# Optimization experiments

Hardware: AMD Instinct MI355X
Metric: run time of the kernel (lower is better)

Reference implementation:

```python
import jax, jax.numpy as jnp
import numpy as np

DIM = 64; NH = 4; WS = (2, 7, 7); FRAMES = 8
# torch code uses head_dim = dim // num_heads for BOTH attentions' scale
SCALE = (DIM // NH) ** -0.5

def _rel_pos_index(ws):
    coords = np.stack(np.meshgrid(np.arange(ws[0]), np.arange(ws[1]), np.arange(ws[2]), indexing='ij'))
    cf = coords.reshape(3, -1)
    rc = (cf[:, :, None] - cf[:, None, :]).transpose(1, 2, 0)
    rc[:, :, 0] += ws[0] - 1; rc[:, :, 1] += ws[1] - 1; rc[:, :, 2] += ws[2] - 1
    rc[:, :, 0] *= (2 * ws[1] - 1) * (2 * ws[2] - 1)
    rc[:, :, 1] *= 2 * ws[2] - 1
    return jnp.asarray(rc.sum(-1))

REL_S = _rel_pos_index(WS)              # (98, 98)
REL_T = _rel_pos_index((FRAMES, 1, 1))  # (8, 8)

def _ln(x, g, b, eps=1e-5):
    m = x.mean(-1, keepdims=True)
    v = ((x - m) ** 2).mean(-1, keepdims=True)
    return (x - m) * jax.lax.rsqrt(v + eps) * g + b

def _conv3d(x, w, b):
    y = jax.lax.conv_general_dilated(x, w, (1, 1, 1), [(1, 1)] * 3,
                                     dimension_numbers=('NCDHW', 'OIDHW', 'NCDHW'))
    return y + b[None, :, None, None, None]

def setup_inputs():
    key = jax.random.key(0)
    ks = jax.random.split(key, 16)
    B, D, H, W, C = 2, 8, 112, 112, DIM
    C2 = C // 2
    n = lambda i, shape: jax.random.normal(ks[i], shape, jnp.float32) * 0.02
    return dict(
        x=jax.random.normal(ks[0], (B, D, H, W, C), jnp.float32),
        mask_matrix=jnp.zeros((1, 98, 98), jnp.float32),
        g1=jnp.ones((C,), jnp.float32), b1=jnp.zeros((C,), jnp.float32),
        rpb_s=n(1, ((2*WS[0]-1)*(2*WS[1]-1)*(2*WS[2]-1), NH)),
        qkv_w_s=n(2, (C, 3*C)), qkv_b_s=jnp.zeros((3*C,), jnp.float32),
        proj_w_s=n(3, (C, C)), proj_b_s=jnp.zeros((C,), jnp.float32),
        rpb_t=n(4, (2*FRAMES-1, NH)),
        qkv_w_t=n(5, (C, 3*C2)), qkv_b_t=jnp.zeros((3*C2,), jnp.float32),
        proj_w_t=n(6, (C2, C)), proj_b_t=jnp.zeros((C,), jnp.float32),
        g2=jnp.ones((C,), jnp.float32), b2=jnp.zeros((C,), jnp.float32),
        p1c1_w=n(7, (C2, C2, 3, 3, 3)), p1c1_b=jnp.zeros((C2,), jnp.float32),
        p1c2_w=n(8, (C2, C2, 3, 3, 3)), p1c2_b=jnp.zeros((C2,), jnp.float32),
        p2c1_w=n(9, (C2, C2, 3, 3, 3)), p2c1_b=jnp.zeros((C2,), jnp.float32),
        p2c2_w=n(10, (C2, C2, 3, 3, 3)), p2c2_b=jnp.zeros((C2,), jnp.float32),
    )

def reference(x, mask_matrix, g1, b1, rpb_s, qkv_w_s, qkv_b_s, proj_w_s, proj_b_s,
              rpb_t, qkv_w_t, qkv_b_t, proj_w_t, proj_b_t, g2, b2,
              p1c1_w, p1c1_b, p1c2_w, p1c2_b, p2c1_w, p2c1_b, p2c2_w, p2c2_b):
    B, D, H, W, C = x.shape
    C2 = C // 2
    wd, wh, ww = WS
    N = wd * wh * ww
    shortcut = x
    h = _ln(x, g1, b1)
    # ---- space attention over (2,7,7) windows (shift=0, H/W/D divisible -> no pad/roll/mask) ----
    xw = h.reshape(B, D // wd, wd, H // wh, wh, W // ww, ww, C)
    xw = xw.transpose(0, 1, 3, 5, 2, 4, 6, 7).reshape(-1, N, C)  # (nW, N, C)
    nw = xw.shape[0]
    qkv = (xw @ qkv_w_s + qkv_b_s).reshape(nw, N, 3, NH, C // NH).transpose(2, 0, 3, 1, 4)
    q, k, v = qkv[0] * SCALE, qkv[1], qkv[2]
    attn = jnp.einsum('whnd,whmd->whnm', q, k)
    bias = rpb_s[REL_S.reshape(-1)].reshape(N, N, NH).transpose(2, 0, 1)
    attn = jax.nn.softmax(attn + bias[None], axis=-1)
    out = jnp.einsum('whnm,whmd->whnd', attn, v).transpose(0, 2, 1, 3).reshape(nw, N, C)
    out = out @ proj_w_s + proj_b_s
    space = out.reshape(B, D // wd, H // wh, W // ww, wd, wh, ww, C)
    space = space.transpose(0, 1, 4, 2, 5, 3, 6, 7).reshape(B, D, H, W, C)
    # ---- time attention over frames (qkv projects to C/2) ----
    xt = h.transpose(0, 2, 3, 1, 4).reshape(B * H * W, D, C)
    qkv_t = (xt @ qkv_w_t + qkv_b_t).reshape(-1, D, 3, NH, C2 // NH).transpose(2, 0, 3, 1, 4)
    qt, kt, vt = qkv_t[0] * SCALE, qkv_t[1], qkv_t[2]
    at = jnp.einsum('bhnd,bhmd->bhnm', qt, kt)
    bias_t = rpb_t[REL_T.reshape(-1)].reshape(D, D, NH).transpose(2, 0, 1)
    at = jax.nn.softmax(at + bias_t[None], axis=-1)
    ot = jnp.einsum('bhnm,bhmd->bhnd', at, vt).transpose(0, 2, 1, 3).reshape(-1, D, C2)
    ot = ot @ proj_w_t + proj_b_t  # (B*H*W, D, C)
    time = ot.reshape(B, H, W, D, C).transpose(0, 3, 1, 2, 4)
    x = shortcut + time + space
    # ---- GRFFNet conv FFN ----
    h2 = _ln(x, g2, b2).transpose(0, 4, 1, 2, 3)  # (B,C,D,H,W)
    x1, x2 = h2[:, :C2], h2[:, C2:]
    y1 = x1 + _conv3d(jax.nn.leaky_relu(_conv3d(x1, p1c1_w, p1c1_b)), p1c2_w, p1c2_b)
    x2 = x2 + y1
    y2 = x2 + _conv3d(jax.nn.leaky_relu(_conv3d(x2, p2c1_w, p2c1_b)), p2c2_w, p2c2_b)
    y = jnp.concatenate([y1, y2], axis=1).transpose(0, 2, 3, 4, 1)
    return x + y
```

## Files before the change

### kernel.cpp

```cpp
#include <hip/hip_runtime.h>
#include <hip/hip_bf16.h>

typedef unsigned short u16;
typedef unsigned int u32;
typedef __attribute__((ext_vector_type(8))) short s16x8;
typedef __attribute__((ext_vector_type(4))) float f32x4;

__device__ __forceinline__ u16 f2b(float v) {
  u32 bits = __float_as_uint(v);
  bits += 0x7fffu + ((bits >> 16) & 1u);
  return (u16)(bits >> 16);
}
__device__ __forceinline__ float b2f(u16 u) { return __uint_as_float(((u32)u) << 16); }
__device__ __forceinline__ float bflo(u32 w) { return __uint_as_float(w << 16); }
__device__ __forceinline__ float bfhi(u32 w) { return __uint_as_float(w & 0xffff0000u); }

__global__ __launch_bounds__(256) void k_ln(const float* __restrict__ x, const float* __restrict__ g,
    const float* __restrict__ b, float* __restrict__ hout, u16* __restrict__ xb) {
  int token = blockIdx.x * 4 + (threadIdx.x >> 6);
  int lane = threadIdx.x & 63;
  long base = (long)token * 64 + lane;
  float v = x[base];
  float s = v;
#pragma unroll
  for (int o = 32; o; o >>= 1) s += __shfl_xor(s, o);
  float m = s * 0.015625f;
  float d = v - m;
  float q = d * d;
#pragma unroll
  for (int o = 32; o; o >>= 1) q += __shfl_xor(q, o);
  float r = rsqrtf(q * 0.015625f + 1e-5f);
  float hv = d * r * g[lane] + b[lane];
  hout[base] = hv;
  if (lane < 32) xb[(long)token * 32 + lane] = f2b(hv);
}

__global__ __launch_bounds__(256) void k_prep(const float* __restrict__ pw, u16* __restrict__ pwb,
    const float* __restrict__ tqw, u16* __restrict__ twb,
    const float* __restrict__ sqw, u16* __restrict__ swb,
    const float* __restrict__ rpb, float* __restrict__ Bt) {
  int i = blockIdx.x * 256 + threadIdx.x;
  if (i < 4096) {
    int r = i & 7, q = i >> 3;
    int col = q & 15; q >>= 4;
    int lk = q & 1; q >>= 1;
    int nt = q & 3, hd = q >> 2;
    pwb[i] = f2b(pw[(hd * 16 + lk * 8 + r) * 64 + nt * 16 + col]);
  } else if (i < 10240) {
    int j = i - 4096;
    int kk = j & 31, q = j >> 5;
    int lm = q & 15, ksnt = q >> 4;
    int ks = ksnt & 1, nt = ksnt >> 1;
    twb[j] = f2b(tqw[(ks * 32 + kk) * 96 + nt * 16 + lm]);
  } else if (i < 22528) {
    int j = i - 10240;
    int kk = j & 31, q = j >> 5;
    int lm = q & 15, ksnt = q >> 4;
    int ks = ksnt & 1, nt = ksnt >> 1;
    swb[j] = f2b(sqw[(ks * 32 + kk) * 192 + nt * 16 + lm]);
  } else {
    int j = i - 22528;
    int m = j % 112, q = j / 112;
    int n = q % 112, hd = q / 112;
    float v = -1e30f;
    if (n < 98 && m < 98) {
      int dzn = n / 49, rn = n % 49, hyn = rn / 7, wxn = rn % 7;
      int dzm = m / 49, rm = m % 49, hym = rm / 7, wxm = rm % 7;
      int idx = (dzn - dzm + 1) * 169 + (hyn - hym + 6) * 13 + (wxn - wxm + 6);
      v = rpb[idx * 4 + hd];
    }
    Bt[j] = v;
  }
}

__global__ __launch_bounds__(256) void k_wprep(const float* __restrict__ w0, const float* __restrict__ w1,
    const float* __restrict__ w2, const float* __restrict__ w3, u16* __restrict__ WB) {
  int j = blockIdx.x * 256 + threadIdx.x;
  int c = j / 27648, j2 = j - c * 27648;
  const float* src = c == 0 ? w0 : c == 1 ? w1 : c == 2 ? w2 : w3;
  int co = j2 / 864, rem = j2 - co * 864, ci = rem / 27, kk = rem - ci * 27;
  WB[c * 27648 + kk * 1024 + co * 32 + ci] = f2b(src[j2]);
}

__global__ __launch_bounds__(256) void k_fused1(const float* __restrict__ x,
    const float* __restrict__ g1, const float* __restrict__ b1,
    const u16* __restrict__ swb, const float* __restrict__ sqb,
    const u16* __restrict__ twb, const float* __restrict__ tqb,
    float* __restrict__ acc, u16* __restrict__ Qg, u16* __restrict__ Kg,
    u16* __restrict__ Vg, u16* __restrict__ T) {
  int l = threadIdx.x & 63, wv = threadIdx.x >> 6;
  int lm = l & 15, lk = l >> 4;
  long t0 = (long)blockIdx.x * 64 + wv * 16;
  long tok = t0 + lm;
  const float* xp = x + tok * 64 + lk * 8;
  float* ap = acc + tok * 64 + lk * 8;
  float va[16];
  float s = 0.f;
#pragma unroll
  for (int ks = 0; ks < 2; ks++) {
    float4 a0 = *(const float4*)(xp + ks * 32);
    float4 a1 = *(const float4*)(xp + ks * 32 + 4);
    *(float4*)(ap + ks * 32) = a0;
    *(float4*)(ap + ks * 32 + 4) = a1;
    va[ks * 8 + 0] = a0.x; va[ks * 8 + 1] = a0.y; va[ks * 8 + 2] = a0.z; va[ks * 8 + 3] = a0.w;
    va[ks * 8 + 4] = a1.x; va[ks * 8 + 5] = a1.y; va[ks * 8 + 6] = a1.z; va[ks * 8 + 7] = a1.w;
    s += a0.x + a0.y + a0.z + a0.w + a1.x + a1.y + a1.z + a1.w;
  }
  s += __shfl_xor(s, 16); s += __shfl_xor(s, 32);
  float m = s * 0.015625f;
  float q = 0.f;
#pragma unroll
  for (int j = 0; j < 16; j++) { float d = va[j] - m; q += d * d; }
  q += __shfl_xor(q, 16); q += __shfl_xor(q, 32);
  float r = rsqrtf(q * 0.015625f + 1e-5f);
  s16x8 A[2];
#pragma unroll
  for (int ks = 0; ks < 2; ks++) {
    float4 g0 = *(const float4*)(g1 + ks * 32 + lk * 8);
    float4 g4 = *(const float4*)(g1 + ks * 32 + lk * 8 + 4);
    float4 c0 = *(const float4*)(b1 + ks * 32 + lk * 8);
    float4 c4 = *(const float4*)(b1 + ks * 32 + lk * 8 + 4);
    s16x8 a;
    a[0] = (short)f2b((va[ks * 8 + 0] - m) * r * g0.x + c0.x);
    a[1] = (short)f2b((va[ks * 8 + 1] - m) * r * g0.y + c0.y);
    a[2] = (short)f2b((va[ks * 8 + 2] - m) * r * g0.z + c0.z);
    a[3] = (short)f2b((va[ks * 8 + 3] - m) * r * g0.w + c0.w);
    a[4] = (short)f2b((va[ks * 8 + 4] - m) * r * g4.x + c4.x);
    a[5] = (short)f2b((va[ks * 8 + 5] - m) * r * g4.y + c4.y);
    a[6] = (short)f2b((va[ks * 8 + 6] - m) * r * g4.z + c4.z);
    a[7] = (short)f2b((va[ks * 8 + 7] - m) * r * g4.w + c4.w);
    A[ks] = a;
  }
  f32x4 C[12], D[6];
#pragma unroll
  for (int nt = 0; nt < 12; nt++) C[nt] = (f32x4){0.f, 0.f, 0.f, 0.f};
#pragma unroll
  for (int nt = 0; nt < 6; nt++) D[nt] = (f32x4){0.f, 0.f, 0.f, 0.f};
#pragma unroll
  for (int ks = 0; ks < 2; ks++) {
#pragma unroll
    for (int nt = 0; nt < 12; nt++) {
      s16x8 B = *(const s16x8*)&swb[((nt * 2 + ks) * 16 + lm) * 32 + lk * 8];
      C[nt] = __builtin_amdgcn_mfma_f32_16x16x32_bf16(A[ks], B, C[nt], 0, 0, 0);
    }
#pragma unroll
    for (int nt = 0; nt < 6; nt++) {
      s16x8 B = *(const s16x8*)&twb[((nt * 2 + ks) * 16 + lm) * 32 + lk * 8];
      D[nt] = __builtin_amdgcn_mfma_f32_16x16x32_bf16(A[ks], B, D[nt], 0, 0, 0);
    }
  }
  float sbv[12], tbv[6];
#pragma unroll
  for (int nt = 0; nt < 12; nt++) sbv[nt] = sqb[nt * 16 + lm];
#pragma unroll
  for (int nt = 0; nt < 6; nt++) tbv[nt] = tqb[nt * 16 + lm];
#pragma unroll
  for (int r4 = 0; r4 < 4; r4++) {
    long t = t0 + lk * 4 + r4;
    int b = (int)(t / 100352); int r1 = (int)(t - (long)b * 100352);
    int d = r1 / 12544; int r2 = r1 - d * 12544;
    int hy = r2 / 112, wx = r2 - hy * 112;
    int d0 = d >> 1, dz = d & 1, h0 = hy / 7, oy = hy - h0 * 7, w0 = wx / 7, ox = wx - w0 * 7;
    int wi = ((b * 4 + d0) * 16 + h0) * 16 + w0;
    int n = dz * 49 + oy * 7 + ox;
    long sbase = (long)(wi * 4) * 1568 + n * 16 + lm;
#pragma unroll
    for (int nt = 0; nt < 12; nt++) {
      int part = nt >> 2, hd = nt & 3;
      float v = C[nt][r4] + sbv[nt];
      long o = sbase + hd * 1568;
      if (part == 0) Qg[o] = f2b(v * 0.25f);
      else if (part == 1) Kg[o] = f2b(v);
      else Vg[o] = f2b(v);
    }
    long sidx = ((long)(b * 12544 + r2) * 8 + d) * 96;
#pragma unroll
    for (int nt = 0; nt < 6; nt++) {
      float v = D[nt][r4] + tbv[nt];
      if (nt < 2) v *= 0.25f;
      T[sidx + nt * 16 + lm] = f2b(v);
    }
  }
}

__global__ __launch_bounds__(512) void k_sattn3(const u16* __restrict__ Qg, const u16* __restrict__ Kg,
    const u16* __restrict__ Vg, const float* __restrict__ Bt, const u16* __restrict__ pwb,
    const float* __restrict__ pb, float* __restrict__ accg) {
  __shared__ __align__(16) u16 sVt[16 * 136];
  __shared__ __align__(16) u16 sP[112 * 120 + 32];
  __shared__ __align__(16) u16 sO[112 * 24];
  int tid = threadIdx.x;
  int wi = blockIdx.x;
  int l = tid & 63, wv = tid >> 6;
  int lm = l & 15, lk = l >> 4;

  for (int i = tid; i < 224; i += 512) { sVt[(i / 14) * 136 + 98 + (i % 14)] = 0; }

  int mt = wv;
  bool act = mt < 7;
  int baserow = mt * 16 + lk * 4;
  int qrow = mt * 16 + lm;
  f32x4 po[4];
#pragma unroll
  for (int b = 0; b < 4; b++) po[b] = (f32x4){0.f, 0.f, 0.f, 0.f};

  for (int hd = 0; hd < 4; hd++) {
    __syncthreads();
    long base = (long)(wi * 4 + hd) * 1568;
    const u32* vp = (const u32*)(Vg + base);
    for (int i = tid; i < 784; i += 512) {
      u32 v = vp[i];
      int n = i >> 3, j2 = (i & 7) * 2;
      sVt[j2 * 136 + n] = (u16)(v & 0xffffu);
      sVt[(j2 + 1) * 136 + n] = (u16)(v >> 16);
    }
    __syncthreads();
    if (!act) continue;

    s16x8 Aq = {};
    if (qrow < 98 && lk < 2) Aq = *(const s16x8*)(Qg + base + qrow * 16 + lk * 8);
    f32x4 S[7];
#pragma unroll
    for (int nt = 0; nt < 7; nt++) {
      int mrow = nt * 16 + lm;
      s16x8 Bk = {};
      if (mrow < 98 && lk < 2) Bk = *(const s16x8*)(Kg + base + mrow * 16 + lk * 8);
      S[nt] = __builtin_amdgcn_mfma_f32_16x16x32_bf16(Aq, Bk, (f32x4){0.f, 0.f, 0.f, 0.f}, 0, 0, 0);
    }
    const float* bt = Bt + hd * 12544 + baserow * 112 + lm;
    float mx0 = -3e38f, mx1 = -3e38f, mx2 = -3e38f, mx3 = -3e38f;
#pragma unroll
    for (int nt = 0; nt < 7; nt++) {
      S[nt][0] += bt[nt * 16];
      S[nt][1] += bt[112 + nt * 16];
      S[nt][2] += bt[224 + nt * 16];
      S[nt][3] += bt[336 + nt * 16];
      mx0 = fmaxf(mx0, S[nt][0]); mx1 = fmaxf(mx1, S[nt][1]);
      mx2 = fmaxf(mx2, S[nt][2]); mx3 = fmaxf(mx3, S[nt][3]);
    }
#pragma unroll
    for (int off = 1; off < 16; off <<= 1) {
      mx0 = fmaxf(mx0, __shfl_xor(mx0, off));
      mx1 = fmaxf(mx1, __shfl_xor(mx1, off));
      mx2 = fmaxf(mx2, __shfl_xor(mx2, off));
      mx3 = fmaxf(mx3, __shfl_xor(mx3, off));
    }
    float s0 = 0.f, s1 = 0.f, s2 = 0.f, s3 = 0.f;
#pragma unroll
    for (int nt = 0; nt < 7; nt++) {
      S[nt][0] = __expf(S[nt][0] - mx0); s0 += S[nt][0];
      S[nt][1] = __expf(S[nt][1] - mx1); s1 += S[nt][1];
      S[nt][2] = __expf(S[nt][2] - mx2); s2 += S[nt][2];
      S[nt][3] = __expf(S[nt][3] - mx3); s3 += S[nt][3];
    }
#pragma unroll
    for (int off = 1; off < 16; off <<= 1) {
      s0 += __shfl_xor(s0, off); s1 += __shfl_xor(s1, off);
      s2 += __shfl_xor(s2, off); s3 += __shfl_xor(s3, off);
    }
    float i0 = 1.f / s0, i1 = 1.f / s1, i2 = 1.f / s2, i3 = 1.f / s3;
#pragma unroll
    for (int nt = 0; nt < 7; nt++) {
      int c = nt * 16 + lm;
      sP[(baserow + 0) * 120 + c] = f2b(S[nt][0] * i0);
      sP[(baserow + 1) * 120 + c] = f2b(S[nt][1] * i1);
      sP[(baserow + 2) * 120 + c] = f2b(S[nt][2] * i2);
      sP[(baserow + 3) * 120 + c] = f2b(S[nt][3] * i3);
    }
    int rowoff = (mt * 16 + lm) * 120;
    f32x4 pv = (f32x4){0.f, 0.f, 0.f, 0.f};
#pragma unroll
    for (int ks = 0; ks < 3; ks++) {
      s16x8 Ap = *(const s16x8*)&sP[rowoff + ks * 32 + lk * 8];
      s16x8 Bv = *(const s16x8*)&sVt[lm * 136 + ks * 32 + lk * 8];
      pv = __builtin_amdgcn_mfma_f32_16x16x32_bf16(Ap, Bv, pv, 0, 0, 0);
    }
    {
      s16x8 Ap = {}, Bv = {};
      if (lk < 2) {
        Ap = *(const s16x8*)&sP[rowoff + 96 + lk * 8];
        Bv = *(const s16x8*)&sVt[lm * 136 + 96 + lk * 8];
      }
      pv = __builtin_amdgcn_mfma_f32_16x16x32_bf16(Ap, Bv, pv, 0, 0, 0);
    }
#pragma unroll
    for (int r = 0; r < 4; r++) sO[(baserow + r) * 24 + lm] = f2b(pv[r]);
    s16x8 Ao = {};
    if (lk < 2) Ao = *(const s16x8*)&sO[(mt * 16 + lm) * 24 + lk * 8];
#pragma unroll
    for (int nt = 0; nt < 4; nt++) {
      s16x8 Bw = {};
      if (lk < 2) Bw = *(const s16x8*)&pwb[((((hd * 4 + nt) * 2 + lk) * 16 + lm) * 8)];
      po[nt] = __builtin_amdgcn_mfma_f32_16x16x32_bf16(Ao, Bw, po[nt], 0, 0, 0);
    }
  }
  if (act) {
    int b = wi >> 10, d0 = (wi >> 8) & 3, h0 = (wi >> 4) & 15, w0 = wi & 15;
    float pbv[4];
#pragma unroll
    for (int nt = 0; nt < 4; nt++) pbv[nt] = pb[nt * 16 + lm];
#pragma unroll
    for (int r = 0; r < 4; r++) {
      int n = mt * 16 + lk * 4 + r;
      if (n >= 98) continue;
      int dz = n / 49, rr = n - dz * 49, oy = rr / 7, ox = rr - oy * 7;
      long p = ((long)(b * 8 + d0 * 2 + dz) * 112 + (h0 * 7 + oy)) * 112 + (w0 * 7 + ox);
      float* ap = accg + p * 64;
#pragma unroll
      for (int nt = 0; nt < 4; nt++) {
        int col = nt * 16 + lm;
        ap[col] += po[nt][r] + pbv[nt];
      }
    }
  }
}

__global__ __launch_bounds__(256) void k_tattn2(const u16* __restrict__ T, const float* __restrict__ rpbt,
    const float* __restrict__ pw, const float* __restrict__ pb, float* __restrict__ acc) {
  __shared__ float sm[4][1064];
  int wv = threadIdx.x >> 6, lane = threadIdx.x & 63;
  int s = blockIdx.x * 4 + wv;
  int b = s / 12544, rr = s - b * 12544;
  float* sq = sm[wv];
  float* o = sq + 800;
  const u32* Tp = (const u32*)(T + (long)s * 768);
  for (int i = lane; i < 192; i += 64) {
    u32 lo = Tp[i * 2], hi = Tp[i * 2 + 1];
    int d = i / 24, base = (i - d * 24) * 4;
    float* dst = sq + d * 100 + base;
    dst[0] = bflo(lo); dst[1] = bfhi(lo); dst[2] = bflo(hi); dst[3] = bfhi(hi);
  }
  __syncthreads();
  if (lane < 32) {
    int hd = lane >> 3, n = lane & 7;
    const float* qr = sq + n * 100 + hd * 8;
    float p[8];
    float mx = -3e38f;
#pragma unroll
    for (int m = 0; m < 8; m++) {
      const float* kr = sq + m * 100 + 32 + hd * 8;
      float sc = 0.f;
#pragma unroll
      for (int e = 0; e < 8; e++) sc += qr[e] * kr[e];
      sc += rpbt[(n - m + 7) * 4 + hd];
      p[m] = sc; mx = fmaxf(mx, sc);
    }
    float sum = 0.f;
#pragma unroll
    for (int m = 0; m < 8; m++) { p[m] = __expf(p[m] - mx); sum += p[m]; }
    float inv = 1.f / sum;
#pragma unroll
    for (int j = 0; j < 8; j++) {
      float oj = 0.f;
#pragma unroll
      for (int m = 0; m < 8; m++) oj += p[m] * sq[m * 100 + 64 + hd * 8 + j];
      o[n * 33 + hd * 8 + j] = oj * inv;
    }
  }
  __syncthreads();
  float a[8];
  float pbc = pb[lane];
#pragma unroll
  for (int n = 0; n < 8; n++) a[n] = pbc;
  for (int k = 0; k < 32; k++) {
    float w = pw[k * 64 + lane];
#pragma unroll
    for (int n = 0; n < 8; n++) a[n] += o[n * 33 + k] * w;
  }
  long base = ((long)b * 100352 + rr) * 64 + lane;
#pragma unroll
  for (int n = 0; n < 8; n++) acc[base + (long)n * 802816] += a[n];
}

__global__ __launch_bounds__(64) void k_convm(const u16* __restrict__ in, const u16* __restrict__ wb,
    const float* __restrict__ bias, int mode,
    const float* __restrict__ hbuf, const float* __restrict__ accb,
    float* __restrict__ dout, float* __restrict__ x2f, u16* __restrict__ outb) {
  int row = blockIdx.x;
  int hh = row % 112, bz = row / 112;
  int d = bz & 7, bb = bz >> 3;
  long prow = (long)row * 112;
  int l = threadIdx.x, lm = l & 15, lk = l >> 4;
  f32x4 acc[7][2];
#pragma unroll
  for (int t = 0; t < 7; t++) { acc[t][0] = (f32x4){0.f,0.f,0.f,0.f}; acc[t][1] = (f32x4){0.f,0.f,0.f,0.f}; }
  for (int kd = 0; kd < 3; kd++) {
    int zd = d + kd - 1;
    if (zd < 0 || zd > 7) continue;
    for (int kh = 0; kh < 3; kh++) {
      int yy = hh + kh - 1;
      if (yy < 0 || yy > 111) continue;
      const u16* ip = in + ((long)((bb * 8 + zd) * 112 + yy)) * 112 * 32;
      int kkb = kd * 9 + kh * 3;
      s16x8 B0[3], B1[3];
#pragma unroll
      for (int kw = 0; kw < 3; kw++) {
        const u16* wp = wb + (kkb + kw) * 1024 + lk * 8;
        B0[kw] = *(const s16x8*)(wp + lm * 32);
        B1[kw] = *(const s16x8*)(wp + (16 + lm) * 32);
      }
#pragma unroll
      for (int t = 0; t < 7; t++) {
#pragma unroll
        for (int kw = 0; kw < 3; kw++) {
          int w = t * 16 + lm + kw - 1;
          s16x8 A = {};
          if ((unsigned)w < 112u) A = *(const s16x8*)(ip + (long)w * 32 + lk * 8);
          acc[t][0] = __builtin_amdgcn_mfma_f32_16x16x32_bf16(A, B0[kw], acc[t][0], 0, 0, 0);
          acc[t][1] = __builtin_amdgcn_mfma_f32_16x16x32_bf16(A, B1[kw], acc[t][1], 0, 0, 0);
        }
      }
    }
  }
  float b0 = bias[lm], b1 = bias[16 + lm];
#pragma unroll
  for (int t = 0; t < 7; t++) {
#pragma unroll
    for (int r = 0; r < 4; r++) {
      long pos = prow + t * 16 + lk * 4 + r;
      float v0 = acc[t][0][r] + b0;
      float v1 = acc[t][1][r] + b1;
      if (mode == 1) {
        v0 = v0 > 0.f ? v0 : 0.01f * v0;
        v1 = v1 > 0.f ? v1 : 0.01f * v1;
        outb[pos * 32 + lm] = f2b(v0);
        outb[pos * 32 + 16 + lm] = f2b(v1);
      } else if (mode == 2) {
        float y0 = v0 + hbuf[pos * 64 + lm];
        float y1v = v1 + hbuf[pos * 64 + 16 + lm];
        dout[pos * 64 + lm] = accb[pos * 64 + lm] + y0;
        dout[pos * 64 + 16 + lm] = accb[pos * 64 + 16 + lm] + y1v;
        float t0 = hbuf[pos * 64 + 32 + lm] + y0;
        float t1 = hbuf[pos * 64 + 48 + lm] + y1v;
        x2f[pos * 32 + lm] = t0;
        x2f[pos * 32 + 16 + lm] = t1;
        outb[pos * 32 + lm] = f2b(t0);
        outb[pos * 32 + 16 + lm] = f2b(t1);
      } else {
        float y0 = v0 + x2f[pos * 32 + lm];
        float y1v = v1 + x2f[pos * 32 + 16 + lm];
        dout[pos * 64 + 32 + lm] = accb[pos * 64 + 32 + lm] + y0;
        dout[pos * 64 + 48 + lm] = accb[pos * 64 + 48 + lm] + y1v;
      }
    }
  }
}

extern "C" void kernel_launch(void* const* d_in, const int* in_sizes, int n_in,
                              void* d_out, int out_size, void* d_ws, size_t ws_size,
                              hipStream_t stream) {
  const float* x        = (const float*)d_in[0];
  const float* g1       = (const float*)d_in[2];
  const float* b1       = (const float*)d_in[3];
  const float* rpb_s    = (const float*)d_in[4];
  const float* qkv_w_s  = (const float*)d_in[5];
  const float* qkv_b_s  = (const float*)d_in[6];
  const float* proj_w_s = (const float*)d_in[7];
  const float* proj_b_s = (const float*)d_in[8];
  const float* rpb_t    = (const float*)d_in[9];
  const float* qkv_w_t  = (const float*)d_in[10];
  const float* qkv_b_t  = (const float*)d_in[11];
  const float* proj_w_t = (const float*)d_in[12];
  const float* proj_b_t = (const float*)d_in[13];
  const float* g2       = (const float*)d_in[14];
  const float* b2       = (const float*)d_in[15];
  const float* c1w = (const float*)d_in[16];
  const float* c1b = (const float*)d_in[17];
  const float* c2w = (const float*)d_in[18];
  const float* c2b = (const float*)d_in[19];
  const float* c3w = (const float*)d_in[20];
  const float* c3b = (const float*)d_in[21];
  const float* c4w = (const float*)d_in[22];
  const float* c4b = (const float*)d_in[23];

  float* acc  = (float*)d_ws;
  float* hbuf = acc + 12845056;
  float* creg = hbuf + 12845056;
  u16* Qg = (u16*)creg;
  u16* Kg = Qg + 12845056;
  u16* Vg = Kg + 12845056;
  u16* Tt = (u16*)hbuf;
  u16* x1b = (u16*)creg;
  u16* t_b = x1b + 6422528;
  u16* x2b = t_b + 6422528;
  float* x2f = (float*)(x2b + 6422528);
  u16* WB = (u16*)(x2f + 6422528);
  float* dout = (float*)d_out;
  u16* pwb = (u16*)d_out;
  u16* twb = (u16*)d_out + 4096;
  u16* swb = (u16*)d_out + 10240;
  float* Bt = (float*)d_out + 11264;

  k_prep<<<284, 256, 0, stream>>>(proj_w_s, pwb, qkv_w_t, twb, qkv_w_s, swb, rpb_s, Bt);
  k_fused1<<<3136, 256, 0, stream>>>(x, g1, b1, swb, qkv_b_s, twb, qkv_b_t,
                                     acc, Qg, Kg, Vg, Tt);
  k_sattn3<<<2048, 512, 0, stream>>>(Qg, Kg, Vg, Bt, pwb, proj_b_s, acc);
  k_wprep<<<432, 256, 0, stream>>>(c1w, c2w, c3w, c4w, WB);
  k_tattn2<<<6272, 256, 0, stream>>>(Tt, rpb_t, proj_w_t, proj_b_t, acc);
  k_ln<<<50176, 256, 0, stream>>>(acc, g2, b2, hbuf, x1b);
  k_convm<<<1792, 64, 0, stream>>>(x1b, WB, c1b, 1, nullptr, nullptr, nullptr, nullptr, t_b);
  k_convm<<<1792, 64, 0, stream>>>(t_b, WB + 27648, c2b, 2, hbuf, acc, dout, x2f, x2b);
  k_convm<<<1792, 64, 0, stream>>>(x2b, WB + 2 * 27648, c3b, 1, nullptr, nullptr, nullptr, nullptr, t_b);
  k_convm<<<1792, 64, 0, stream>>>(t_b, WB + 3 * 27648, c4b, 4, nullptr, acc, dout, x2f, nullptr);
}
```

Measured before the change: 452.0 us.

## Fuse LayerNorm2 into time attention, stage Q/K in LDS, drop fp32 residual buffers

Removes the separate LayerNorm kernel by computing the second LayerNorm at the end of the time-attention kernel. It writes bf16 halves x1b/x2h directly, so the fp32 hbuf and x2f buffers are no longer written or re-read by the conv kernels, cutting a full-tensor read/write pass. The spatial attention kernel now loads Q and K into shared memory, padded with zero rows, instead of reading them per-MFMA from global memory. The conv residuals now come from bf16 copies rather than fp32, which slightly reduces accuracy of the residual path.

```diff
diff --git a/kernel.cpp b/kernel.cpp
--- a/kernel.cpp
+++ b/kernel.cpp
@@ -14,26 +14,6 @@
 __device__ __forceinline__ float b2f(u16 u) { return __uint_as_float(((u32)u) << 16); }
 __device__ __forceinline__ float bflo(u32 w) { return __uint_as_float(w << 16); }
 __device__ __forceinline__ float bfhi(u32 w) { return __uint_as_float(w & 0xffff0000u); }
-
-__global__ __launch_bounds__(256) void k_ln(const float* __restrict__ x, const float* __restrict__ g,
-    const float* __restrict__ b, float* __restrict__ hout, u16* __restrict__ xb) {
-  int token = blockIdx.x * 4 + (threadIdx.x >> 6);
-  int lane = threadIdx.x & 63;
-  long base = (long)token * 64 + lane;
-  float v = x[base];
-  float s = v;
-#pragma unroll
-  for (int o = 32; o; o >>= 1) s += __shfl_xor(s, o);
-  float m = s * 0.015625f;
-  float d = v - m;
-  float q = d * d;
-#pragma unroll
-  for (int o = 32; o; o >>= 1) q += __shfl_xor(q, o);
-  float r = rsqrtf(q * 0.015625f + 1e-5f);
-  float hv = d * r * g[lane] + b[lane];
-  hout[base] = hv;
-  if (lane < 32) xb[(long)token * 32 + lane] = f2b(hv);
-}
 
 __global__ __launch_bounds__(256) void k_prep(const float* __restrict__ pw, u16* __restrict__ pwb,
     const float* __restrict__ tqw, u16* __restrict__ twb,
@@ -186,6 +166,8 @@
 __global__ __launch_bounds__(512) void k_sattn3(const u16* __restrict__ Qg, const u16* __restrict__ Kg,
     const u16* __restrict__ Vg, const float* __restrict__ Bt, const u16* __restrict__ pwb,
     const float* __restrict__ pb, float* __restrict__ accg) {
+  __shared__ __align__(16) u16 sQ[112 * 24];
+  __shared__ __align__(16) u16 sK[112 * 24];
   __shared__ __align__(16) u16 sVt[16 * 136];
   __shared__ __align__(16) u16 sP[112 * 120 + 32];
   __shared__ __align__(16) u16 sO[112 * 24];
@@ -194,12 +176,12 @@
   int l = tid & 63, wv = tid >> 6;
   int lm = l & 15, lk = l >> 4;
 
+  for (int i = tid; i < 336; i += 512) { sQ[2352 + i] = 0; sK[2352 + i] = 0; }
   for (int i = tid; i < 224; i += 512) { sVt[(i / 14) * 136 + 98 + (i % 14)] = 0; }
 
   int mt = wv;
   bool act = mt < 7;
   int baserow = mt * 16 + lk * 4;
-  int qrow = mt * 16 + lm;
   f32x4 po[4];
 #pragma unroll
   for (int b = 0; b < 4; b++) po[b] = (f32x4){0.f, 0.f, 0.f, 0.f};
@@ -207,7 +189,19 @@
   for (int hd = 0; hd < 4; hd++) {
     __syncthreads();
     long base = (long)(wi * 4 + hd) * 1568;
+    const u32* qp = (const u32*)(Qg + base);
+    const u32* kp = (const u32*)(Kg + base);
     const u32* vp = (const u32*)(Vg + base);
+    for (int i = tid; i < 784; i += 512) {
+      u32 v = qp[i];
+      int n = i >> 3, j2 = (i & 7) * 2;
+      *(u32*)&sQ[n * 24 + j2] = v;
+    }
+    for (int i = tid; i < 784; i += 512) {
+      u32 v = kp[i];
+      int n = i >> 3, j2 = (i & 7) * 2;
+      *(u32*)&sK[n * 24 + j2] = v;
+    }
     for (int i = tid; i < 784; i += 512) {
       u32 v = vp[i];
       int n = i >> 3, j2 = (i & 7) * 2;
@@ -218,13 +212,12 @@
     if (!act) continue;
 
     s16x8 Aq = {};
-    if (qrow < 98 && lk < 2) Aq = *(const s16x8*)(Qg + base + qrow * 16 + lk * 8);
+    if (lk < 2) Aq = *(const s16x8*)&sQ[(mt * 16 + lm) * 24 + lk * 8];
     f32x4 S[7];
 #pragma unroll
     for (int nt = 0; nt < 7; nt++) {
-      int mrow = nt * 16 + lm;
       s16x8 Bk = {};
-      if (mrow < 98 && lk < 2) Bk = *(const s16x8*)(Kg + base + mrow * 16 + lk * 8);
+      if (lk < 2) Bk = *(const s16x8*)&sK[(nt * 16 + lm) * 24 + lk * 8];
       S[nt] = __builtin_amdgcn_mfma_f32_16x16x32_bf16(Aq, Bk, (f32x4){0.f, 0.f, 0.f, 0.f}, 0, 0, 0);
     }
     const float* bt = Bt + hd * 12544 + baserow * 112 + lm;
@@ -315,8 +308,10 @@
   }
 }
 
-__global__ __launch_bounds__(256) void k_tattn2(const u16* __restrict__ T, const float* __restrict__ rpbt,
-    const float* __restrict__ pw, const float* __restrict__ pb, float* __restrict__ acc) {
+__global__ __launch_bounds__(256) void k_tattn3(const u16* __restrict__ T, const float* __restrict__ rpbt,
+    const float* __restrict__ pw, const float* __restrict__ pb,
+    const float* __restrict__ g2, const float* __restrict__ b2,
+    float* __restrict__ acc, u16* __restrict__ x1b, u16* __restrict__ x2h) {
   __shared__ float sm[4][1064];
   int wv = threadIdx.x >> 6, lane = threadIdx.x & 63;
   int s = blockIdx.x * 4 + wv;
@@ -367,15 +362,35 @@
 #pragma unroll
     for (int n = 0; n < 8; n++) a[n] += o[n * 33 + k] * w;
   }
+  float gv = g2[lane], bv = b2[lane];
   long base = ((long)b * 100352 + rr) * 64 + lane;
-#pragma unroll
-  for (int n = 0; n < 8; n++) acc[base + (long)n * 802816] += a[n];
+  long pos0 = (long)b * 100352 + rr;
+#pragma unroll
+  for (int n = 0; n < 8; n++) {
+    long ai = base + (long)n * 802816;
+    float av = acc[ai] + a[n];
+    acc[ai] = av;
+    float sum = av;
+#pragma unroll
+    for (int off = 32; off; off >>= 1) sum += __shfl_xor(sum, off);
+    float mean = sum * 0.015625f;
+    float d = av - mean;
+    float q = d * d;
+#pragma unroll
+    for (int off = 32; off; off >>= 1) q += __shfl_xor(q, off);
+    float r = rsqrtf(q * 0.015625f + 1e-5f);
+    float hv = d * r * gv + bv;
+    long pos = pos0 + (long)n * 12544;
+    u16 hb = f2b(hv);
+    if (lane < 32) x1b[pos * 32 + lane] = hb;
+    else x2h[pos * 32 + lane - 32] = hb;
+  }
 }
 
 __global__ __launch_bounds__(64) void k_convm(const u16* __restrict__ in, const u16* __restrict__ wb,
     const float* __restrict__ bias, int mode,
-    const float* __restrict__ hbuf, const float* __restrict__ accb,
-    float* __restrict__ dout, float* __restrict__ x2f, u16* __restrict__ outb) {
+    const u16* __restrict__ res1, const u16* __restrict__ res2,
+    const float* __restrict__ accb, float* __restrict__ dout, u16* __restrict__ outb) {
   int row = blockIdx.x;
   int hh = row % 112, bz = row / 112;
   int d = bz & 7, bb = bz >> 3;
@@ -426,19 +441,17 @@
         outb[pos * 32 + lm] = f2b(v0);
         outb[pos * 32 + 16 + lm] = f2b(v1);
       } else if (mode == 2) {
-        float y0 = v0 + hbuf[pos * 64 + lm];
-        float y1v = v1 + hbuf[pos * 64 + 16 + lm];
+        float y0 = v0 + b2f(res1[pos * 32 + lm]);
+        float y1v = v1 + b2f(res1[pos * 32 + 16 + lm]);
         dout[pos * 64 + lm] = accb[pos * 64 + lm] + y0;
         dout[pos * 64 + 16 + lm] = accb[pos * 64 + 16 + lm] + y1v;
-        float t0 = hbuf[pos * 64 + 32 + lm] + y0;
-        float t1 = hbuf[pos * 64 + 48 + lm] + y1v;
-        x2f[pos * 32 + lm] = t0;
-        x2f[pos * 32 + 16 + lm] = t1;
+        float t0 = b2f(res2[pos * 32 + lm]) + y0;
+        float t1 = b2f(res2[pos * 32 + 16 + lm]) + y1v;
         outb[pos * 32 + lm] = f2b(t0);
         outb[pos * 32 + 16 + lm] = f2b(t1);
       } else {
-        float y0 = v0 + x2f[pos * 32 + lm];
-        float y1v = v1 + x2f[pos * 32 + 16 + lm];
+        float y0 = v0 + b2f(res1[pos * 32 + lm]);
+        float y1v = v1 + b2f(res1[pos * 32 + 16 + lm]);
         dout[pos * 64 + 32 + lm] = accb[pos * 64 + 32 + lm] + y0;
         dout[pos * 64 + 48 + lm] = accb[pos * 64 + 48 + lm] + y1v;
       }
@@ -483,8 +496,8 @@
   u16* x1b = (u16*)creg;
   u16* t_b = x1b + 6422528;
   u16* x2b = t_b + 6422528;
-  float* x2f = (float*)(x2b + 6422528);
-  u16* WB = (u16*)(x2f + 6422528);
+  u16* x2h = x2b + 6422528;
+  u16* WB  = x2h + 6422528;
   float* dout = (float*)d_out;
   u16* pwb = (u16*)d_out;
   u16* twb = (u16*)d_out + 4096;
@@ -496,10 +509,9 @@
                                      acc, Qg, Kg, Vg, Tt);
   k_sattn3<<<2048, 512, 0, stream>>>(Qg, Kg, Vg, Bt, pwb, proj_b_s, acc);
   k_wprep<<<432, 256, 0, stream>>>(c1w, c2w, c3w, c4w, WB);
-  k_tattn2<<<6272, 256, 0, stream>>>(Tt, rpb_t, proj_w_t, proj_b_t, acc);
-  k_ln<<<50176, 256, 0, stream>>>(acc, g2, b2, hbuf, x1b);
+  k_tattn3<<<6272, 256, 0, stream>>>(Tt, rpb_t, proj_w_t, proj_b_t, g2, b2, acc, x1b, x2h);
   k_convm<<<1792, 64, 0, stream>>>(x1b, WB, c1b, 1, nullptr, nullptr, nullptr, nullptr, t_b);
-  k_convm<<<1792, 64, 0, stream>>>(t_b, WB + 27648, c2b, 2, hbuf, acc, dout, x2f, x2b);
+  k_convm<<<1792, 64, 0, stream>>>(t_b, WB + 27648, c2b, 2, x1b, x2h, acc, dout, x2b);
   k_convm<<<1792, 64, 0, stream>>>(x2b, WB + 2 * 27648, c3b, 1, nullptr, nullptr, nullptr, nullptr, t_b);
-  k_convm<<<1792, 64, 0, stream>>>(t_b, WB + 3 * 27648, c4b, 4, nullptr, acc, dout, x2f, nullptr);
-}
+  k_convm<<<1792, 64, 0, stream>>>(t_b, WB + 3 * 27648, c4b, 4, x2b, nullptr, acc, dout, nullptr);
+}
```

Result: slower. 571.1 us (+26.3%).
